# Optimization experiments

Measured on AMD Instinct MI355X. Metric: run time of the kernel, lower is better.

The kernel has to match this reference:

```python
import jax, jax.numpy as jnp
import numpy as np

B, L1, L2 = 4, 1024, 512
D_PG, D_EX = 2304, 1024
H, HKV, DH = 8, 4, 256
SCALE = 256.0 ** -0.5


def _rope(x, cos, sin):
    # x: [B, L, h, DH]; cos/sin: [B, L, 1, DH//2]
    x = x.astype(jnp.float32)
    x1, x2 = jnp.split(x, 2, axis=-1)
    return jnp.concatenate([x1 * cos - x2 * sin, x2 * cos + x1 * sin], axis=-1)


def setup_inputs() -> dict:
    key = jax.random.key(0)
    ks = jax.random.split(key, 16)
    s = 0.02
    return {
        "pg_embeds": jax.random.normal(ks[0], (B, L1, D_PG), jnp.float32),
        "ex_embeds": jax.random.normal(ks[1], (B, L2, D_EX), jnp.float32),
        "cos": jax.random.normal(ks[2], (B, L1 + L2, 1, DH // 2), jnp.float32),
        "sin": jax.random.normal(ks[3], (B, L1 + L2, 1, DH // 2), jnp.float32),
        "attention_mask": jnp.zeros((B, L1 + L2, L1 + L2), jnp.float32),
        "Wq0": jax.random.normal(ks[4], (H * DH, D_PG), jnp.float32) * s,
        "Wk0": jax.random.normal(ks[5], (HKV * DH, D_PG), jnp.float32) * s,
        "Wv0": jax.random.normal(ks[6], (HKV * DH, D_PG), jnp.float32) * s,
        "Wo0": jax.random.normal(ks[7], (D_PG, H * DH), jnp.float32) * s,
        "Wq1": jax.random.normal(ks[8], (H * DH, D_EX), jnp.float32) * s,
        "Wk1": jax.random.normal(ks[9], (HKV * DH, D_EX), jnp.float32) * s,
        "Wv1": jax.random.normal(ks[10], (HKV * DH, D_EX), jnp.float32) * s,
        "Wo1": jax.random.normal(ks[11], (D_EX, H * DH), jnp.float32) * s,
    }


def reference(pg_embeds, ex_embeds, cos, sin, attention_mask,
              Wq0, Wk0, Wv0, Wo0, Wq1, Wk1, Wv1, Wo1):
    b, l1 = pg_embeds.shape[0], pg_embeds.shape[1]
    l2 = ex_embeds.shape[1]
    # per-stream QKV projections, then concat along sequence
    q = jnp.concatenate([
        (pg_embeds @ Wq0.T).reshape(b, l1, H, DH),
        (ex_embeds @ Wq1.T).reshape(b, l2, H, DH)], axis=1)
    k = jnp.concatenate([
        (pg_embeds @ Wk0.T).reshape(b, l1, HKV, DH),
        (ex_embeds @ Wk1.T).reshape(b, l2, HKV, DH)], axis=1)
    v = jnp.concatenate([
        (pg_embeds @ Wv0.T).reshape(b, l1, HKV, DH),
        (ex_embeds @ Wv1.T).reshape(b, l2, HKV, DH)], axis=1)
    q = _rope(q, cos, sin)  # fp32
    k = _rope(k, cos, sin)
    # GQA: repeat KV heads to match query heads
    rep = H // HKV
    k = jnp.repeat(k, rep, axis=2)
    v = jnp.repeat(jnp.repeat(v, rep, axis=2).astype(jnp.float32), 1, axis=0)
    # scores: [B, H, L, L]
    scores = jnp.einsum('bqhd,bkhd->bhqk', q, k) * SCALE
    scores = scores + attention_mask[:, None, :, :]
    p = jax.nn.softmax(scores, axis=-1)
    att = jnp.einsum('bhqk,bkhd->bqhd', p, v).reshape(b, l1 + l2, H * DH)
    out0 = att[:, :l1] @ Wo0.T
    out1 = att[:, l1:] @ Wo1.T
    return (out0, out1)
```

## Files before the change

kernel.cpp:

```cpp
#include <hip/hip_runtime.h>
#include <stdint.h>
#include <stddef.h>


typedef _Float16 f16;
typedef _Float16 f16x8 __attribute__((ext_vector_type(8)));
typedef _Float16 f16x4 __attribute__((ext_vector_type(4)));
typedef float    f32x4 __attribute__((ext_vector_type(4)));

__device__ __forceinline__ void async_ld16(const void* g, void* l) {
  __builtin_amdgcn_global_load_lds((const __attribute__((address_space(1))) void*)g,
                                   (__attribute__((address_space(3))) void*)l,
                                   16, 0, 0);
}

template <typename Epi>
__device__ __forceinline__ void gemm_core(f16* At, f16* Bt,
                                          const f16* __restrict__ A, int lda,
                                          const f16* __restrict__ Bm, int ldb,
                                          int K, Epi&& epi)
{
  const int t    = threadIdx.x;
  const int w    = t >> 6;
  const int lane = t & 63;
  const int q4   = lane >> 4;
  const int l16  = lane & 15;
  const int wm   = w >> 1;
  const int wn   = w & 1;

  const f32x4 vzero = {0.f, 0.f, 0.f, 0.f};
  f32x4 acc[4][4];
#pragma unroll
  for (int i = 0; i < 4; ++i)
#pragma unroll
    for (int j = 0; j < 4; ++j) acc[i][j] = vzero;

  const int srow = t >> 2;
  const int scol = (t & 3) << 3;
  const f16* aP = A  + (size_t)srow * lda + scol;
  const f16* bP = Bm + (size_t)srow * ldb + scol;
  f16* ldsA0 = At + w * 512;
  f16* ldsA1 = At + 2048 + w * 512;
  f16* ldsB0 = Bt + w * 512;
  f16* ldsB1 = Bt + 2048 + w * 512;
  const size_t a64 = (size_t)64 * lda;
  const size_t b64 = (size_t)64 * ldb;

  for (int k0 = 0; k0 < K; k0 += 32) {
    async_ld16(aP + k0,        ldsA0);
    async_ld16(aP + a64 + k0,  ldsA1);
    async_ld16(bP + k0,        ldsB0);
    async_ld16(bP + b64 + k0,  ldsB1);
    __syncthreads();

    f16x8 af[4], bf[4];
#pragma unroll
    for (int mi = 0; mi < 4; ++mi)
      af[mi] = *(const f16x8*)(At + (wm * 64 + mi * 16 + l16) * 32 + q4 * 8);
#pragma unroll
    for (int ni = 0; ni < 4; ++ni)
      bf[ni] = *(const f16x8*)(Bt + (wn * 64 + ni * 16 + l16) * 32 + q4 * 8);

#pragma unroll
    for (int mi = 0; mi < 4; ++mi)
#pragma unroll
      for (int ni = 0; ni < 4; ++ni)
        acc[mi][ni] = __builtin_amdgcn_mfma_f32_16x16x32_f16(af[mi], bf[ni], acc[mi][ni], 0, 0, 0);
    __syncthreads();
  }

#pragma unroll
  for (int mi = 0; mi < 4; ++mi)
#pragma unroll
    for (int ni = 0; ni < 4; ++ni)
#pragma unroll
      for (int r = 0; r < 4; ++r)
        epi(wm * 64 + mi * 16 + q4 * 4 + r, wn * 64 + ni * 16 + l16, acc[mi][ni][r]);
}

__global__ __launch_bounds__(256) void k_qkv(
    const f16* __restrict__ xpg, const f16* __restrict__ xex,
    const f16* __restrict__ W0,  const f16* __restrict__ W1,
    f16* __restrict__ q, f16* __restrict__ k, f16* __restrict__ v)
{
  __shared__ alignas(16) f16 At[128 * 32];
  __shared__ alignas(16) f16 Bt[128 * 32];
  const int idx = blockIdx.x;
  const bool s0 = idx < 1024;
  int by, bx, K;
  const f16 *A, *B;
  if (s0) { by = idx >> 5; bx = idx & 31; K = 2304;
            A = xpg + (size_t)by * 128 * 2304; B = W0 + (size_t)bx * 128 * 2304; }
  else    { int j = idx - 1024; by = j >> 5; bx = j & 31; K = 1024;
            A = xex + (size_t)by * 128 * 1024; B = W1 + (size_t)bx * 128 * 1024; }
  const int rowbase = by * 128, colbase = bx * 128;
  gemm_core(At, Bt, A, K, B, K, K, [&](int r, int c, float fv) {
    int m = rowbase + r;
    int row = s0 ? ((m >> 10) * 1536 + (m & 1023))
                 : ((m >> 9) * 1536 + 1024 + (m & 511));
    int col = colbase + c;
    f16 h = (f16)fv;
    if      (col < 2048) q[(size_t)row * 2048 + col]        = h;
    else if (col < 3072) k[(size_t)row * 1024 + col - 2048] = h;
    else                 v[(size_t)row * 1024 + col - 3072] = h;
  });
}

__global__ __launch_bounds__(256) void k_post(
    f16* __restrict__ q, f16* __restrict__ k,
    const float* __restrict__ cs, const float* __restrict__ sn,
    const float* __restrict__ msk, f16* __restrict__ mkh,
    const f16* __restrict__ v, f16* __restrict__ vt)
{
  const int blk = blockIdx.x;
  if (blk < 6144) {
    __shared__ f16 tile[32][33];
    const int b = blk / 1536, r0 = blk % 1536;
    const int d0 = (r0 & 31) * 32, l0 = (r0 >> 5) * 32;
    const int t = threadIdx.x;
    const int tr = t >> 5, tc = t & 31;
#pragma unroll
    for (int i = 0; i < 4; ++i)
      tile[tr + i * 8][tc] = v[((size_t)b * 1536 + l0 + tr + i * 8) * 1024 + d0 + tc];
    __syncthreads();
#pragma unroll
    for (int i = 0; i < 4; ++i) {
      int d = d0 + tr + i * 8;
      vt[(((size_t)b * 4 + (d >> 8)) * 256 + (d & 255)) * 1536 + l0 + tc] = tile[tc][tr + i * 8];
    }
  } else if (blk < 15360) {
    const size_t gid = ((size_t)(blk - 6144) * 256 + threadIdx.x) * 4;
    float4 m4 = *(const float4*)(msk + gid);
    f16x4 o = {(f16)m4.x, (f16)m4.y, (f16)m4.z, (f16)m4.w};
    *(f16x4*)(mkh + gid) = o;
  } else {
    const size_t tid8 = ((size_t)(blk - 15360) * 256 + threadIdx.x) * 8;
    f16* base; size_t row; int col;
    if (tid8 < 12582912ull) { base = q + tid8; row = tid8 >> 11; col = (int)(tid8 & 2047); }
    else { size_t f = tid8 - 12582912ull; base = k + f; row = f >> 10; col = (int)(f & 1023); }
    const int j0 = (col & 255) >> 1;
    f16x8 x = *(const f16x8*)base;
    float4 c4 = *(const float4*)(cs + row * 128 + j0);
    float4 s4 = *(const float4*)(sn + row * 128 + j0);
    f16x8 o;
    const float cc[4] = {c4.x, c4.y, c4.z, c4.w};
    const float ss[4] = {s4.x, s4.y, s4.z, s4.w};
#pragma unroll
    for (int p = 0; p < 4; ++p) {
      float x1 = (float)x[2 * p], x2 = (float)x[2 * p + 1];
      o[2 * p]     = (f16)(x1 * cc[p] - x2 * ss[p]);
      o[2 * p + 1] = (f16)(x2 * cc[p] + x1 * ss[p]);
    }
    *(f16x8*)base = o;
  }
}

__global__ __launch_bounds__(256) void k_attn(
    const f16* __restrict__ qb, const f16* __restrict__ kb,
    const f16* __restrict__ mask, f16* __restrict__ Sdst,
    const f16* __restrict__ Psrc, const f16* __restrict__ vt,
    f16* __restrict__ att0, f16* __restrict__ att1,
    const f16* __restrict__ wo0, const f16* __restrict__ wo1,
    float* __restrict__ out0, float* __restrict__ out1,
    int b_sc, int b_pv, int b_op, int npv, int nop)
{
  __shared__ alignas(16) f16 At[128 * 32];
  __shared__ alignas(16) f16 Bt[128 * 32];
  const int idx = blockIdx.x;
  if (idx < nop) {
    int by, bx, ldc; const f16 *A, *B; float* C;
    if (idx < 144) { by = b_op * 8 + idx / 18; bx = idx % 18;
                     A = att0 + (size_t)by * 128 * 2048; B = wo0 + (size_t)bx * 128 * 2048;
                     C = out0; ldc = 2304; }
    else           { int j = idx - 144; by = b_op * 4 + (j >> 3); bx = j & 7;
                     A = att1 + (size_t)by * 128 * 2048; B = wo1 + (size_t)bx * 128 * 2048;
                     C = out1; ldc = 1024; }
    const int rowbase = by * 128, colbase = bx * 128;
    gemm_core(At, Bt, A, 2048, B, 2048, 2048, [&](int r, int c, float fv) {
      C[(size_t)(rowbase + r) * ldc + colbase + c] = fv;
    });
  } else if (idx < nop + npv) {
    const int j = idx - nop;
    const int h = j / 24, rem = j % 24, by = rem >> 1, bx = rem & 1;
    const f16* A = Psrc + (size_t)h * 1536 * 1536 + (size_t)by * 128 * 1536;
    const f16* B = vt + (size_t)(b_pv * 4 + (h >> 1)) * 256 * 1536 + (size_t)bx * 128 * 1536;
    const int rowbase = by * 128, colbase = bx * 128;
    gemm_core(At, Bt, A, 1536, B, 1536, 1536, [&](int r, int c, float fv) {
      int m = rowbase + r;
      if (m < 1024) att0[((size_t)(b_pv * 1024 + m))       * 2048 + h * 256 + colbase + c] = (f16)fv;
      else          att1[((size_t)(b_pv * 512 + m - 1024)) * 2048 + h * 256 + colbase + c] = (f16)fv;
    });
  } else {
    const int j = idx - nop - npv;
    const int h = j / 144, rem = j % 144, by = rem / 12, bx = rem % 12;
    const f16* A = qb + (size_t)b_sc * 1536 * 2048 + h * 256 + (size_t)by * 128 * 2048;
    const f16* B = kb + (size_t)b_sc * 1536 * 1024 + (h >> 1) * 256 + (size_t)bx * 128 * 1024;
    f16* Sz = Sdst + (size_t)h * 1536 * 1536;
    const f16* mb = mask + (size_t)b_sc * 1536 * 1536;
    const int rowbase = by * 128, colbase = bx * 128;
    gemm_core(At, Bt, A, 2048, B, 1024, 256, [&](int r, int c, float fv) {
      size_t i = (size_t)(rowbase + r) * 1536 + colbase + c;
      Sz[i] = (f16)(fv * 0.0625f + (float)mb[i]);
    });
  }
}

__global__ __launch_bounds__(256) void k_softmax(f16* __restrict__ S)
{
  const int row = blockIdx.x * 4 + (threadIdx.x >> 6);
  const int lane = threadIdx.x & 63;
  f16* p = S + (size_t)row * 1536 + lane * 8;
  f16x8 v0 = *(const f16x8*)p;
  f16x8 v1 = *(const f16x8*)(p + 512);
  f16x8 v2 = *(const f16x8*)(p + 1024);
  float x[24];
#pragma unroll
  for (int i = 0; i < 8; ++i) {
    x[i] = (float)v0[i]; x[8 + i] = (float)v1[i]; x[16 + i] = (float)v2[i];
  }
  float mx = x[0];
#pragma unroll
  for (int i = 1; i < 24; ++i) mx = fmaxf(mx, x[i]);
#pragma unroll
  for (int o = 32; o > 0; o >>= 1) mx = fmaxf(mx, __shfl_xor(mx, o, 64));
  float s = 0.f;
#pragma unroll
  for (int i = 0; i < 24; ++i) { x[i] = __expf(x[i] - mx); s += x[i]; }
#pragma unroll
  for (int o = 32; o > 0; o >>= 1) s += __shfl_xor(s, o, 64);
  const float inv = 1.f / s;
  f16x8 o0, o1, o2;
#pragma unroll
  for (int i = 0; i < 8; ++i) {
    o0[i] = (f16)(x[i] * inv); o1[i] = (f16)(x[8 + i] * inv); o2[i] = (f16)(x[16 + i] * inv);
  }
  *(f16x8*)p = o0; *(f16x8*)(p + 512) = o1; *(f16x8*)(p + 1024) = o2;
}

__global__ __launch_bounds__(256) void k_cast_all(
    const float* __restrict__ s0, const float* __restrict__ s1,
    const float* __restrict__ s2, const float* __restrict__ s3,
    const float* __restrict__ s4, const float* __restrict__ s5,
    f16* __restrict__ ws)
{
  const size_t gid = ((size_t)blockIdx.x * 256 + threadIdx.x) * 4;
  const float* s; size_t off, dst;
  if      (gid < 9437184ull)  { s = s0; off = gid;               dst = 0ull        + off; }
  else if (gid < 11534336ull) { s = s1; off = gid - 9437184ull;  dst = 9437184ull  + off; }
  else if (gid < 13893632ull) { s = s2; off = gid - 11534336ull; dst = 18612224ull + off; }
  else if (gid < 18612224ull) { s = s3; off = gid - 13893632ull; dst = 20971520ull + off; }
  else if (gid < 19660800ull) { s = s4; off = gid - 18612224ull; dst = 28835840ull + off; }
  else                        { s = s5; off = gid - 19660800ull; dst = 29884416ull + off; }
  float4 v = *(const float4*)(s + off);
  f16x4 o = {(f16)v.x, (f16)v.y, (f16)v.z, (f16)v.w};
  *(f16x4*)(ws + dst) = o;
}

__global__ __launch_bounds__(256) void k_cast_wr(
    const float* __restrict__ wq0, const float* __restrict__ wk0,
    const float* __restrict__ wq1, const float* __restrict__ wk1,
    f16* __restrict__ W0c, f16* __restrict__ W1c)
{
  const int idx = blockIdx.x;
  const float* src; f16* dstm; int K, r, drow;
  if      (idx < 2048) { src = wq0; dstm = W0c; K = 2304; r = idx;        drow = idx; }
  else if (idx < 3072) { src = wk0; dstm = W0c; K = 2304; r = idx - 2048; drow = idx; }
  else if (idx < 5120) { src = wq1; dstm = W1c; K = 1024; r = idx - 3072; drow = idx - 3072; }
  else                 { src = wk1; dstm = W1c; K = 1024; r = idx - 5120; drow = idx - 3072; }
  const int w = r & 255;
  const int srow = (r & ~255) + (w >> 1) + ((w & 1) << 7);
  const float* sp = src + (size_t)srow * K;
  f16* dp = dstm + (size_t)drow * K;
  for (int c = threadIdx.x * 4; c < K; c += 1024) {
    float4 v = *(const float4*)(sp + c);
    f16x4 o = {(f16)v.x, (f16)v.y, (f16)v.z, (f16)v.w};
    *(f16x4*)(dp + c) = o;
  }
}

extern "C" void kernel_launch(void* const* d_in, const int* in_sizes, int n_in,
                              void* d_out, int out_size, void* d_ws, size_t ws_size,
                              hipStream_t stream)
{
  (void)in_sizes; (void)n_in; (void)out_size; (void)ws_size;
  const float* pg  = (const float*)d_in[0];
  const float* ex  = (const float*)d_in[1];
  const float* cs  = (const float*)d_in[2];
  const float* sn  = (const float*)d_in[3];
  const float* msk = (const float*)d_in[4];

  char* ws = (char*)d_ws;
  f16* xpg  = (f16*)(ws + 0);
  f16* xex  = (f16*)(ws + 18874368);
  f16* W0c  = (f16*)(ws + 23068672);
  f16* wo0c = (f16*)(ws + 41943040);
  f16* W1c  = (f16*)(ws + 51380224);
  f16* wo1c = (f16*)(ws + 59768832);
  f16* qb   = (f16*)(ws + 63963136);
  f16* kb   = (f16*)(ws + 89128960);
  f16* vb   = (f16*)(ws + 101711872);
  f16* vt   = (f16*)(ws + 114294784);
  f16* att0 = (f16*)(ws + 126877696);
  f16* att1 = (f16*)(ws + 143654912);
  f16* S0   = (f16*)(ws + 152043520);
  f16* S1   = (f16*)(ws + 189792256);
  f16* mkh  = W0c;
  float* out0 = (float*)d_out;
  float* out1 = out0 + 9437184;

  k_cast_all<<<21248, 256, 0, stream>>>(
      pg, ex, (const float*)d_in[7], (const float*)d_in[8],
      (const float*)d_in[11], (const float*)d_in[12], (f16*)ws);
  k_cast_wr<<<6144, 256, 0, stream>>>(
      (const float*)d_in[5], (const float*)d_in[6],
      (const float*)d_in[9], (const float*)d_in[10], W0c, W1c);

  k_qkv<<<1536, 256, 0, stream>>>(xpg, xex, W0c, W1c, qb, kb, vb);

  k_post<<<24576, 256, 0, stream>>>(qb, kb, cs, sn, msk, mkh, vb, vt);

  k_attn<<<1152, 256, 0, stream>>>(qb, kb, mkh, S0, S0, vt, att0, att1, wo0c, wo1c, out0, out1, 0, 0, 0, 0, 0);
  k_softmax<<<3072, 256, 0, stream>>>(S0);
  k_attn<<<1344, 256, 0, stream>>>(qb, kb, mkh, S1, S0, vt, att0, att1, wo0c, wo1c, out0, out1, 1, 0, 0, 192, 0);
  k_softmax<<<3072, 256, 0, stream>>>(S1);
  k_attn<<<1520, 256, 0, stream>>>(qb, kb, mkh, S0, S1, vt, att0, att1, wo0c, wo1c, out0, out1, 2, 1, 0, 192, 176);
  k_softmax<<<3072, 256, 0, stream>>>(S0);
  k_attn<<<1520, 256, 0, stream>>>(qb, kb, mkh, S1, S0, vt, att0, att1, wo0c, wo1c, out0, out1, 3, 2, 1, 192, 176);
  k_softmax<<<3072, 256, 0, stream>>>(S1);

  k_attn<<<368, 256, 0, stream>>>(qb, kb, mkh, S0, S1, vt, att0, att1, wo0c, wo1c, out0, out1, 0, 3, 2, 192, 176);
  k_attn<<<176, 256, 0, stream>>>(qb, kb, mkh, S0, S1, vt, att0, att1, wo0c, wo1c, out0, out1, 0, 0, 3, 0, 176);
}
```

Before: 682.7 us.

## Rewrite QKV GEMM with 256x128 tiles, double-buffered async LDS loads

Replaces the QKV projection kernel with a 512-thread, 256x128-tile GEMM that double-buffers A and B tiles in LDS through async global-to-LDS loads, interleaved with MFMA phases and raised wave priority. It is meant to hide global load latency behind matrix math and to reuse the weight tiles across more rows. The epilogue now picks the q, k or v destination once per block instead of branching per element. The larger LDS footprint and 512-thread blocks may limit occupancy, and the hand-placed vmcnt waits and barriers must be exactly right or the results will be wrong.

```diff
diff --git a/kernel.cpp b/kernel.cpp
--- a/kernel.cpp
+++ b/kernel.cpp
@@ -78,32 +78,155 @@
         epi(wm * 64 + mi * 16 + q4 * 4 + r, wn * 64 + ni * 16 + l16, acc[mi][ni][r]);
 }
 
-__global__ __launch_bounds__(256) void k_qkv(
+__global__ __launch_bounds__(512, 2) void k_qkv2(
     const f16* __restrict__ xpg, const f16* __restrict__ xex,
     const f16* __restrict__ W0,  const f16* __restrict__ W1,
     f16* __restrict__ q, f16* __restrict__ k, f16* __restrict__ v)
 {
-  __shared__ alignas(16) f16 At[128 * 32];
-  __shared__ alignas(16) f16 Bt[128 * 32];
-  const int idx = blockIdx.x;
-  const bool s0 = idx < 1024;
-  int by, bx, K;
-  const f16 *A, *B;
+  __shared__ alignas(16) f16 lds[49152];
+  const int idx  = blockIdx.x;
+  const int t    = threadIdx.x;
+  const int w    = t >> 6;
+  const int lane = t & 63;
+  const int q4   = lane >> 4;
+  const int l16  = lane & 15;
+  const int wm   = w >> 1;
+  const int wn   = w & 1;
+
+  int by, bx, K; const f16 *A, *B;
+  const bool s0 = idx < 512;
   if (s0) { by = idx >> 5; bx = idx & 31; K = 2304;
-            A = xpg + (size_t)by * 128 * 2304; B = W0 + (size_t)bx * 128 * 2304; }
-  else    { int j = idx - 1024; by = j >> 5; bx = j & 31; K = 1024;
-            A = xex + (size_t)by * 128 * 1024; B = W1 + (size_t)bx * 128 * 1024; }
-  const int rowbase = by * 128, colbase = bx * 128;
-  gemm_core(At, Bt, A, K, B, K, K, [&](int r, int c, float fv) {
-    int m = rowbase + r;
-    int row = s0 ? ((m >> 10) * 1536 + (m & 1023))
-                 : ((m >> 9) * 1536 + 1024 + (m & 511));
-    int col = colbase + c;
-    f16 h = (f16)fv;
-    if      (col < 2048) q[(size_t)row * 2048 + col]        = h;
-    else if (col < 3072) k[(size_t)row * 1024 + col - 2048] = h;
-    else                 v[(size_t)row * 1024 + col - 3072] = h;
-  });
+            A = xpg + (size_t)by * 256 * 2304; B = W0 + (size_t)bx * 128 * 2304; }
+  else    { int j = idx - 512; by = j >> 5; bx = j & 31; K = 1024;
+            A = xex + (size_t)by * 256 * 1024; B = W1 + (size_t)bx * 128 * 1024; }
+
+  const int srow = w * 16 + (lane >> 2);
+  const int scol = (lane & 3) * 8;
+  const f16* aP = A + (size_t)srow * K + scol;
+  const f16* bP = B + (size_t)srow * K + scol;
+  const size_t a128 = (size_t)128 * K;
+  const int wl = w * 512;
+
+  const int arow = (wm * 64 + l16) * 32 + q4 * 8;
+  const int brow = (wn * 64 + l16) * 32 + q4 * 8;
+
+  f32x4 acc[4][4];
+  const f32x4 vz = {0.f, 0.f, 0.f, 0.f};
+#pragma unroll
+  for (int i = 0; i < 4; ++i)
+#pragma unroll
+    for (int j = 0; j < 4; ++j) acc[i][j] = vz;
+
+  async_ld16(aP,              lds + wl);
+  async_ld16(aP + a128,       lds + 4096 + wl);
+  async_ld16(bP,              lds + 32768 + wl);
+  asm volatile("" ::: "memory");
+  async_ld16(aP + 32,         lds + 8192 + wl);
+  async_ld16(aP + a128 + 32,  lds + 8192 + 4096 + wl);
+  async_ld16(bP + 32,         lds + 32768 + 4096 + wl);
+  asm volatile("s_waitcnt vmcnt(3)" ::: "memory");
+  asm volatile("s_barrier" ::: "memory");
+
+  const int NT = K >> 6;
+  int cb = 0;
+  for (int tk = 0; tk < NT; ++tk) {
+    f16* aT = lds + cb * 16384;
+    f16* bT = lds + 32768 + cb * 8192;
+    f16* aD = lds + (cb ^ 1) * 16384;
+    f16* bD = lds + 32768 + (cb ^ 1) * 8192;
+    const int kn = (tk + 1) << 6;
+    const bool st = tk < NT - 1;
+    f16x8 bf[4];
+
+    {
+      f16x8 A0 = *(const f16x8*)(aT + arow);
+      f16x8 A1 = *(const f16x8*)(aT + arow + 512);
+#pragma unroll
+      for (int ni = 0; ni < 4; ++ni)
+        bf[ni] = *(const f16x8*)(bT + brow + ni * 512);
+      if (st) { async_ld16(aP + kn,        aD + wl);
+                async_ld16(aP + a128 + kn, aD + 4096 + wl); }
+      asm volatile("s_barrier" ::: "memory");
+      __builtin_amdgcn_s_setprio(1);
+#pragma unroll
+      for (int ni = 0; ni < 4; ++ni)
+        acc[0][ni] = __builtin_amdgcn_mfma_f32_16x16x32_f16(A0, bf[ni], acc[0][ni], 0, 0, 0);
+#pragma unroll
+      for (int ni = 0; ni < 4; ++ni)
+        acc[1][ni] = __builtin_amdgcn_mfma_f32_16x16x32_f16(A1, bf[ni], acc[1][ni], 0, 0, 0);
+      __builtin_amdgcn_s_setprio(0);
+      asm volatile("s_barrier" ::: "memory");
+    }
+    {
+      f16x8 A0 = *(const f16x8*)(aT + arow + 1024);
+      f16x8 A1 = *(const f16x8*)(aT + arow + 1536);
+      if (st) { async_ld16(bP + kn, bD + wl);
+                asm volatile("s_waitcnt vmcnt(3)" ::: "memory"); }
+      else    { asm volatile("s_waitcnt vmcnt(0)" ::: "memory"); }
+      asm volatile("s_barrier" ::: "memory");
+      __builtin_amdgcn_s_setprio(1);
+#pragma unroll
+      for (int ni = 0; ni < 4; ++ni)
+        acc[2][ni] = __builtin_amdgcn_mfma_f32_16x16x32_f16(A0, bf[ni], acc[2][ni], 0, 0, 0);
+#pragma unroll
+      for (int ni = 0; ni < 4; ++ni)
+        acc[3][ni] = __builtin_amdgcn_mfma_f32_16x16x32_f16(A1, bf[ni], acc[3][ni], 0, 0, 0);
+      __builtin_amdgcn_s_setprio(0);
+      asm volatile("s_barrier" ::: "memory");
+    }
+    {
+      f16x8 A0 = *(const f16x8*)(aT + 8192 + arow);
+      f16x8 A1 = *(const f16x8*)(aT + 8192 + arow + 512);
+#pragma unroll
+      for (int ni = 0; ni < 4; ++ni)
+        bf[ni] = *(const f16x8*)(bT + 4096 + brow + ni * 512);
+      if (st) { async_ld16(aP + kn + 32,        aD + 8192 + wl);
+                async_ld16(aP + a128 + kn + 32, aD + 8192 + 4096 + wl); }
+      asm volatile("s_barrier" ::: "memory");
+      __builtin_amdgcn_s_setprio(1);
+#pragma unroll
+      for (int ni = 0; ni < 4; ++ni)
+        acc[0][ni] = __builtin_amdgcn_mfma_f32_16x16x32_f16(A0, bf[ni], acc[0][ni], 0, 0, 0);
+#pragma unroll
+      for (int ni = 0; ni < 4; ++ni)
+        acc[1][ni] = __builtin_amdgcn_mfma_f32_16x16x32_f16(A1, bf[ni], acc[1][ni], 0, 0, 0);
+      __builtin_amdgcn_s_setprio(0);
+      asm volatile("s_barrier" ::: "memory");
+    }
+    {
+      f16x8 A0 = *(const f16x8*)(aT + 8192 + arow + 1024);
+      f16x8 A1 = *(const f16x8*)(aT + 8192 + arow + 1536);
+      if (st) { async_ld16(bP + kn + 32, bD + 4096 + wl);
+                asm volatile("s_waitcnt vmcnt(3)" ::: "memory"); }
+      asm volatile("s_barrier" ::: "memory");
+      __builtin_amdgcn_s_setprio(1);
+#pragma unroll
+      for (int ni = 0; ni < 4; ++ni)
+        acc[2][ni] = __builtin_amdgcn_mfma_f32_16x16x32_f16(A0, bf[ni], acc[2][ni], 0, 0, 0);
+#pragma unroll
+      for (int ni = 0; ni < 4; ++ni)
+        acc[3][ni] = __builtin_amdgcn_mfma_f32_16x16x32_f16(A1, bf[ni], acc[3][ni], 0, 0, 0);
+      __builtin_amdgcn_s_setprio(0);
+      asm volatile("s_barrier" ::: "memory");
+    }
+    cb ^= 1;
+  }
+
+  f16* D; int ldd, coff;
+  if (bx < 16)      { D = q; ldd = 2048; coff = 0; }
+  else if (bx < 24) { D = k; ldd = 1024; coff = 2048; }
+  else              { D = v; ldd = 1024; coff = 3072; }
+  const int colb = bx * 128 + wn * 64 - coff + l16;
+  int rowb = s0 ? ((by >> 2) * 1536 + (by & 3) * 256)
+                : ((by >> 1) * 1536 + 1024 + (by & 1) * 256);
+  rowb += wm * 64 + q4 * 4;
+#pragma unroll
+  for (int mi = 0; mi < 4; ++mi)
+#pragma unroll
+    for (int ni = 0; ni < 4; ++ni)
+#pragma unroll
+      for (int r = 0; r < 4; ++r)
+        D[(size_t)(rowb + mi * 16 + r) * ldd + colb + ni * 16] = (f16)acc[mi][ni][r];
 }
 
 __global__ __launch_bounds__(256) void k_post(
@@ -315,7 +438,7 @@
       (const float*)d_in[5], (const float*)d_in[6],
       (const float*)d_in[9], (const float*)d_in[10], W0c, W1c);
 
-  k_qkv<<<1536, 256, 0, stream>>>(xpg, xex, W0c, W1c, qb, kb, vb);
+  k_qkv2<<<768, 512, 0, stream>>>(xpg, xex, W0c, W1c, qb, kb, vb);
 
   k_post<<<24576, 256, 0, stream>>>(qb, kb, cs, sn, msk, mkh, vb, vt);
 
```

Measured after the change: 662.2 us. -3.0%, faster.

## Double-buffer GEMM core with async LDS prefetch and larger 256x128 tiles

Applied to the files above, without the earlier changes.

Replaces the single-stage GEMM core with a double-buffered pipeline. Global-to-LDS async loads for the next 64-wide K step are issued while MFMAs run on the current step, and waitcnt, barriers and setprio interleave the two. Blocks grow to 512 threads computing 256x128 tiles, which halves the grid of the QKV, score, PV and output-projection launches. This is meant to hide memory latency and raise operand reuse, at the cost of much higher LDS use (96KB per block), which limits occupancy.

```diff
diff --git a/kernel.cpp b/kernel.cpp
--- a/kernel.cpp
+++ b/kernel.cpp
@@ -15,10 +15,10 @@
 }
 
 template <typename Epi>
-__device__ __forceinline__ void gemm_core(f16* At, f16* Bt,
-                                          const f16* __restrict__ A, int lda,
-                                          const f16* __restrict__ Bm, int ldb,
-                                          int K, Epi&& epi)
+__device__ __forceinline__ void gemm_pipe(f16* lds,
+    const f16* __restrict__ A, int lda,
+    const f16* __restrict__ B, int ldb,
+    int K, Epi&& epi)
 {
   const int t    = threadIdx.x;
   const int w    = t >> 6;
@@ -28,45 +28,77 @@
   const int wm   = w >> 1;
   const int wn   = w & 1;
 
-  const f32x4 vzero = {0.f, 0.f, 0.f, 0.f};
+  const int srow = w * 16 + (lane >> 2);
+  const int scol = (lane & 3) * 8;
+  const f16* aP = A + (size_t)srow * lda + scol;
+  const f16* bP = B + (size_t)srow * ldb + scol;
+  const size_t a128 = (size_t)128 * lda;
+  const int wl = w * 512;
+
+  const int arow = (wm * 64 + l16) * 32 + q4 * 8;
+  const int brow = (wn * 64 + l16) * 32 + q4 * 8;
+
   f32x4 acc[4][4];
+  const f32x4 vz = {0.f, 0.f, 0.f, 0.f};
 #pragma unroll
   for (int i = 0; i < 4; ++i)
 #pragma unroll
-    for (int j = 0; j < 4; ++j) acc[i][j] = vzero;
-
-  const int srow = t >> 2;
-  const int scol = (t & 3) << 3;
-  const f16* aP = A  + (size_t)srow * lda + scol;
-  const f16* bP = Bm + (size_t)srow * ldb + scol;
-  f16* ldsA0 = At + w * 512;
-  f16* ldsA1 = At + 2048 + w * 512;
-  f16* ldsB0 = Bt + w * 512;
-  f16* ldsB1 = Bt + 2048 + w * 512;
-  const size_t a64 = (size_t)64 * lda;
-  const size_t b64 = (size_t)64 * ldb;
-
-  for (int k0 = 0; k0 < K; k0 += 32) {
-    async_ld16(aP + k0,        ldsA0);
-    async_ld16(aP + a64 + k0,  ldsA1);
-    async_ld16(bP + k0,        ldsB0);
-    async_ld16(bP + b64 + k0,  ldsB1);
-    __syncthreads();
-
-    f16x8 af[4], bf[4];
-#pragma unroll
-    for (int mi = 0; mi < 4; ++mi)
-      af[mi] = *(const f16x8*)(At + (wm * 64 + mi * 16 + l16) * 32 + q4 * 8);
-#pragma unroll
-    for (int ni = 0; ni < 4; ++ni)
-      bf[ni] = *(const f16x8*)(Bt + (wn * 64 + ni * 16 + l16) * 32 + q4 * 8);
-
-#pragma unroll
-    for (int mi = 0; mi < 4; ++mi)
-#pragma unroll
-      for (int ni = 0; ni < 4; ++ni)
-        acc[mi][ni] = __builtin_amdgcn_mfma_f32_16x16x32_f16(af[mi], bf[ni], acc[mi][ni], 0, 0, 0);
-    __syncthreads();
+    for (int j = 0; j < 4; ++j) acc[i][j] = vz;
+
+  async_ld16(aP,             lds + wl);
+  async_ld16(aP + a128,      lds + 4096 + wl);
+  async_ld16(bP,             lds + 32768 + wl);
+  asm volatile("" ::: "memory");
+  async_ld16(aP + 32,        lds + 8192 + wl);
+  async_ld16(aP + a128 + 32, lds + 8192 + 4096 + wl);
+  async_ld16(bP + 32,        lds + 32768 + 4096 + wl);
+  asm volatile("s_waitcnt vmcnt(3)" ::: "memory");
+  asm volatile("s_barrier" ::: "memory");
+
+  const int NT = K >> 6;
+  int cb = 0;
+  for (int tk = 0; tk < NT; ++tk) {
+    f16* aT = lds + cb * 16384;
+    f16* bT = lds + 32768 + cb * 8192;
+    f16* aD = lds + (cb ^ 1) * 16384;
+    f16* bD = lds + 32768 + (cb ^ 1) * 8192;
+    const int kn = (tk + 1) << 6;
+    const bool st = tk < NT - 1;
+#pragma unroll
+    for (int s = 0; s < 2; ++s) {
+      const f16* aS = aT + s * 8192;
+      const f16* bS = bT + s * 4096;
+      f16x8 af[4], bf[4];
+#pragma unroll
+      for (int i = 0; i < 4; ++i) {
+        af[i] = *(const f16x8*)(aS + arow + i * 512);
+        bf[i] = *(const f16x8*)(bS + brow + i * 512);
+      }
+      if (st) {
+        if (s == 0) {
+          async_ld16(aP + kn,        aD + wl);
+          async_ld16(aP + a128 + kn, aD + 4096 + wl);
+          async_ld16(bP + kn,        bD + wl);
+        } else {
+          async_ld16(aP + kn + 32,        aD + 8192 + wl);
+          async_ld16(aP + a128 + kn + 32, aD + 8192 + 4096 + wl);
+          async_ld16(bP + kn + 32,        bD + 4096 + wl);
+        }
+        asm volatile("s_waitcnt vmcnt(3)" ::: "memory");
+      } else if (s == 0) {
+        asm volatile("s_waitcnt vmcnt(0)" ::: "memory");
+      }
+      asm volatile("s_barrier" ::: "memory");
+      __builtin_amdgcn_s_setprio(1);
+#pragma unroll
+      for (int mi = 0; mi < 4; ++mi)
+#pragma unroll
+        for (int ni = 0; ni < 4; ++ni)
+          acc[mi][ni] = __builtin_amdgcn_mfma_f32_16x16x32_f16(af[mi], bf[ni], acc[mi][ni], 0, 0, 0);
+      __builtin_amdgcn_s_setprio(0);
+      asm volatile("s_barrier" ::: "memory");
+    }
+    cb ^= 1;
   }
 
 #pragma unroll
@@ -78,31 +110,30 @@
         epi(wm * 64 + mi * 16 + q4 * 4 + r, wn * 64 + ni * 16 + l16, acc[mi][ni][r]);
 }
 
-__global__ __launch_bounds__(256) void k_qkv(
+__global__ __launch_bounds__(512, 2) void k_qkv3(
     const f16* __restrict__ xpg, const f16* __restrict__ xex,
     const f16* __restrict__ W0,  const f16* __restrict__ W1,
     f16* __restrict__ q, f16* __restrict__ k, f16* __restrict__ v)
 {
-  __shared__ alignas(16) f16 At[128 * 32];
-  __shared__ alignas(16) f16 Bt[128 * 32];
+  __shared__ alignas(16) f16 lds[49152];
   const int idx = blockIdx.x;
-  const bool s0 = idx < 1024;
-  int by, bx, K;
-  const f16 *A, *B;
+  int by, bx, K; const f16 *A, *B;
+  const bool s0 = idx < 512;
   if (s0) { by = idx >> 5; bx = idx & 31; K = 2304;
-            A = xpg + (size_t)by * 128 * 2304; B = W0 + (size_t)bx * 128 * 2304; }
-  else    { int j = idx - 1024; by = j >> 5; bx = j & 31; K = 1024;
-            A = xex + (size_t)by * 128 * 1024; B = W1 + (size_t)bx * 128 * 1024; }
-  const int rowbase = by * 128, colbase = bx * 128;
-  gemm_core(At, Bt, A, K, B, K, K, [&](int r, int c, float fv) {
-    int m = rowbase + r;
-    int row = s0 ? ((m >> 10) * 1536 + (m & 1023))
-                 : ((m >> 9) * 1536 + 1024 + (m & 511));
-    int col = colbase + c;
-    f16 h = (f16)fv;
-    if      (col < 2048) q[(size_t)row * 2048 + col]        = h;
-    else if (col < 3072) k[(size_t)row * 1024 + col - 2048] = h;
-    else                 v[(size_t)row * 1024 + col - 3072] = h;
+            A = xpg + (size_t)by * 256 * 2304; B = W0 + (size_t)bx * 128 * 2304; }
+  else    { int j = idx - 512; by = j >> 5; bx = j & 31; K = 1024;
+            A = xex + (size_t)by * 256 * 1024; B = W1 + (size_t)bx * 128 * 1024; }
+
+  f16* D; int ldd, coff;
+  if (bx < 16)      { D = q; ldd = 2048; coff = 0; }
+  else if (bx < 24) { D = k; ldd = 1024; coff = 2048; }
+  else              { D = v; ldd = 1024; coff = 3072; }
+  const int colb = bx * 128 - coff;
+  const int rowb = s0 ? ((by >> 2) * 1536 + (by & 3) * 256)
+                      : ((by >> 1) * 1536 + 1024 + (by & 1) * 256);
+
+  gemm_pipe(lds, A, K, B, K, K, [&](int r, int c, float fv) {
+    D[(size_t)(rowb + r) * ldd + colb + c] = (f16)fv;
   });
 }
 
@@ -155,7 +186,7 @@
   }
 }
 
-__global__ __launch_bounds__(256) void k_attn(
+__global__ __launch_bounds__(512, 2) void k_attn2(
     const f16* __restrict__ qb, const f16* __restrict__ kb,
     const f16* __restrict__ mask, f16* __restrict__ Sdst,
     const f16* __restrict__ Psrc, const f16* __restrict__ vt,
@@ -164,42 +195,42 @@
     float* __restrict__ out0, float* __restrict__ out1,
     int b_sc, int b_pv, int b_op, int npv, int nop)
 {
-  __shared__ alignas(16) f16 At[128 * 32];
-  __shared__ alignas(16) f16 Bt[128 * 32];
+  __shared__ alignas(16) f16 lds[49152];
   const int idx = blockIdx.x;
   if (idx < nop) {
-    int by, bx, ldc; const f16 *A, *B; float* C;
-    if (idx < 144) { by = b_op * 8 + idx / 18; bx = idx % 18;
-                     A = att0 + (size_t)by * 128 * 2048; B = wo0 + (size_t)bx * 128 * 2048;
-                     C = out0; ldc = 2304; }
-    else           { int j = idx - 144; by = b_op * 4 + (j >> 3); bx = j & 7;
-                     A = att1 + (size_t)by * 128 * 2048; B = wo1 + (size_t)bx * 128 * 2048;
-                     C = out1; ldc = 1024; }
-    const int rowbase = by * 128, colbase = bx * 128;
-    gemm_core(At, Bt, A, 2048, B, 2048, 2048, [&](int r, int c, float fv) {
-      C[(size_t)(rowbase + r) * ldc + colbase + c] = fv;
+    int by, bx, ldc, rowb; const f16 *A, *B; float* C;
+    if (idx < 72) { by = idx / 18; bx = idx % 18;
+                    A = att0 + (size_t)(b_op * 4 + by) * 256 * 2048;
+                    B = wo0 + (size_t)bx * 128 * 2048;
+                    C = out0; ldc = 2304; rowb = b_op * 1024 + by * 256; }
+    else          { int j = idx - 72; by = j >> 3; bx = j & 7;
+                    A = att1 + (size_t)(b_op * 2 + by) * 256 * 2048;
+                    B = wo1 + (size_t)bx * 128 * 2048;
+                    C = out1; ldc = 1024; rowb = b_op * 512 + by * 256; }
+    const int colb = bx * 128;
+    gemm_pipe(lds, A, 2048, B, 2048, 2048, [&](int r, int c, float fv) {
+      C[(size_t)(rowb + r) * ldc + colb + c] = fv;
     });
   } else if (idx < nop + npv) {
     const int j = idx - nop;
-    const int h = j / 24, rem = j % 24, by = rem >> 1, bx = rem & 1;
-    const f16* A = Psrc + (size_t)h * 1536 * 1536 + (size_t)by * 128 * 1536;
+    const int h = j / 12, rem = j % 12, by = rem >> 1, bx = rem & 1;
+    const f16* A = Psrc + (size_t)h * 1536 * 1536 + (size_t)by * 256 * 1536;
     const f16* B = vt + (size_t)(b_pv * 4 + (h >> 1)) * 256 * 1536 + (size_t)bx * 128 * 1536;
-    const int rowbase = by * 128, colbase = bx * 128;
-    gemm_core(At, Bt, A, 1536, B, 1536, 1536, [&](int r, int c, float fv) {
-      int m = rowbase + r;
-      if (m < 1024) att0[((size_t)(b_pv * 1024 + m))       * 2048 + h * 256 + colbase + c] = (f16)fv;
-      else          att1[((size_t)(b_pv * 512 + m - 1024)) * 2048 + h * 256 + colbase + c] = (f16)fv;
+    f16* dst = (by < 4)
+      ? att0 + (size_t)(b_pv * 1024 + by * 256) * 2048 + h * 256 + bx * 128
+      : att1 + (size_t)(b_pv * 512 + (by - 4) * 256) * 2048 + h * 256 + bx * 128;
+    gemm_pipe(lds, A, 1536, B, 1536, 1536, [&](int r, int c, float fv) {
+      dst[(size_t)r * 2048 + c] = (f16)fv;
     });
   } else {
     const int j = idx - nop - npv;
-    const int h = j / 144, rem = j % 144, by = rem / 12, bx = rem % 12;
-    const f16* A = qb + (size_t)b_sc * 1536 * 2048 + h * 256 + (size_t)by * 128 * 2048;
+    const int h = j / 72, rem = j % 72, by = rem / 12, bx = rem % 12;
+    const f16* A = qb + (size_t)b_sc * 1536 * 2048 + h * 256 + (size_t)by * 256 * 2048;
     const f16* B = kb + (size_t)b_sc * 1536 * 1024 + (h >> 1) * 256 + (size_t)bx * 128 * 1024;
-    f16* Sz = Sdst + (size_t)h * 1536 * 1536;
-    const f16* mb = mask + (size_t)b_sc * 1536 * 1536;
-    const int rowbase = by * 128, colbase = bx * 128;
-    gemm_core(At, Bt, A, 2048, B, 1024, 256, [&](int r, int c, float fv) {
-      size_t i = (size_t)(rowbase + r) * 1536 + colbase + c;
+    f16* Sz = Sdst + (size_t)h * 1536 * 1536 + (size_t)by * 256 * 1536 + bx * 128;
+    const f16* mb = mask + (size_t)b_sc * 1536 * 1536 + (size_t)by * 256 * 1536 + bx * 128;
+    gemm_pipe(lds, A, 2048, B, 1024, 256, [&](int r, int c, float fv) {
+      size_t i = (size_t)r * 1536 + c;
       Sz[i] = (f16)(fv * 0.0625f + (float)mb[i]);
     });
   }
@@ -315,19 +346,19 @@
       (const float*)d_in[5], (const float*)d_in[6],
       (const float*)d_in[9], (const float*)d_in[10], W0c, W1c);
 
-  k_qkv<<<1536, 256, 0, stream>>>(xpg, xex, W0c, W1c, qb, kb, vb);
+  k_qkv3<<<768, 512, 0, stream>>>(xpg, xex, W0c, W1c, qb, kb, vb);
 
   k_post<<<24576, 256, 0, stream>>>(qb, kb, cs, sn, msk, mkh, vb, vt);
 
-  k_attn<<<1152, 256, 0, stream>>>(qb, kb, mkh, S0, S0, vt, att0, att1, wo0c, wo1c, out0, out1, 0, 0, 0, 0, 0);
+  k_attn2<<<576, 512, 0, stream>>>(qb, kb, mkh, S0, S0, vt, att0, att1, wo0c, wo1c, out0, out1, 0, 0, 0, 0, 0);
   k_softmax<<<3072, 256, 0, stream>>>(S0);
-  k_attn<<<1344, 256, 0, stream>>>(qb, kb, mkh, S1, S0, vt, att0, att1, wo0c, wo1c, out0, out1, 1, 0, 0, 192, 0);
+  k_attn2<<<672, 512, 0, stream>>>(qb, kb, mkh, S1, S0, vt, att0, att1, wo0c, wo1c, out0, out1, 1, 0, 0, 96, 0);
   k_softmax<<<3072, 256, 0, stream>>>(S1);
-  k_attn<<<1520, 256, 0, stream>>>(qb, kb, mkh, S0, S1, vt, att0, att1, wo0c, wo1c, out0, out1, 2, 1, 0, 192, 176);
+  k_attn2<<<760, 512, 0, stream>>>(qb, kb, mkh, S0, S1, vt, att0, att1, wo0c, wo1c, out0, out1, 2, 1, 0, 96, 88);
   k_softmax<<<3072, 256, 0, stream>>>(S0);
-  k_attn<<<1520, 256, 0, stream>>>(qb, kb, mkh, S1, S0, vt, att0, att1, wo0c, wo1c, out0, out1, 3, 2, 1, 192, 176);
+  k_attn2<<<760, 512, 0, stream>>>(qb, kb, mkh, S1, S0, vt, att0, att1, wo0c, wo1c, out0, out1, 3, 2, 1, 96, 88);
   k_softmax<<<3072, 256, 0, stream>>>(S1);
 
-  k_attn<<<368, 256, 0, stream>>>(qb, kb, mkh, S0, S1, vt, att0, att1, wo0c, wo1c, out0, out1, 0, 3, 2, 192, 176);
-  k_attn<<<176, 256, 0, stream>>>(qb, kb, mkh, S0, S1, vt, att0, att1, wo0c, wo1c, out0, out1, 0, 0, 3, 0, 176);
-}
+  k_attn2<<<184, 512, 0, stream>>>(qb, kb, mkh, S0, S1, vt, att0, att1, wo0c, wo1c, out0, out1, 0, 3, 2, 96, 88);
+  k_attn2<<<88, 512, 0, stream>>>(qb, kb, mkh, S0, S1, vt, att0, att1, wo0c, wo1c, out0, out1, 0, 0, 3, 0, 88);
+}
```

Result: faster. 649.2 us (-4.9%).
